# Optimization experiments

Hardware: AMD Instinct MI355X
Metric: run time of the kernel (lower is better)

The kernel has to match this reference:

```python
import jax, jax.numpy as jnp
import numpy as np
from jax import lax

SIZE = 20          # lattice half-extent in Angstrom
R = SIZE * 2       # 40 voxels per side (0.5 A pitch)
ROT = (1, 2, 3)    # fixed rot90 multiplicities (original draws randint(0,4,size=3))


def setup_inputs() -> dict:
    key = jax.random.key(0)
    ks = jax.random.split(key, 8)
    B, N1, N2, F = 8, 400, 64, 54
    # atom coordinates roughly inside the 20A box centered on the pocket
    pos1 = (jax.random.uniform(ks[0], (B, N1, 3)) - 0.5) * 18.0
    pos2 = (jax.random.uniform(ks[1], (B, N2, 3)) - 0.5) * 18.0
    h1 = jax.random.uniform(ks[2], (B, N1, F))
    h2 = jax.random.uniform(ks[3], (B, N2, F))
    valid1 = jnp.ones((B, N1), jnp.float32)
    valid2 = jnp.ones((B, N2), jnp.float32)
    conv_w = jax.random.normal(ks[4], (128, F, 3, 3, 3)) * 0.05
    conv_b = jnp.zeros((128,), jnp.float32)
    fc_w = jax.random.normal(ks[5], (128 * R * R * R, 1)) * 1e-3
    fc_b = jnp.zeros((1,), jnp.float32)
    return dict(pos1=pos1, pos2=pos2, h1=h1, h2=h2, valid1=valid1,
                valid2=valid2, conv_w=conv_w, conv_b=conv_b,
                fc_w=fc_w, fc_b=fc_b)


def _scatter_one(lat, idx, feat):
    # lat: [R+1,R+1,R+1,F] (extra slot R is the dump cell for out-of-range atoms)
    inb = jnp.all((idx >= 0) & (idx <= R - 1), axis=-1)          # [N]
    idxc = jnp.where(inb[:, None], idx, R)                       # route invalid -> R
    return lat.at[idxc[:, 0], idxc[:, 1], idxc[:, 2]].set(feat)


def _forward(pos1, pos2, h1, h2, valid1, valid2, conv_w, conv_b, fc_w, fc_b):
    B, _, F = h1.shape
    h1 = h1 * valid1[..., None]
    h2 = h2 * valid2[..., None]
    pos1 = pos1 * valid1[..., None]
    pos2 = pos2 * valid2[..., None]
    # per-batch bounding box of non-zero pos1 atoms -> box center `sub`
    nz = (pos1.sum(-1) == 0)[..., None]                          # [B,N1,1]
    bmax = jnp.max(pos1 + jnp.where(nz, -1e10, 0.0), axis=1)
    bmin = jnp.min(pos1 + jnp.where(nz, 1e10, 0.0), axis=1)
    sub = (bmin + (bmax - bmin) / 2)[:, None, :]                 # [B,1,3]
    half = jnp.float32(SIZE / 2)
    idx1 = jnp.floor((pos1 - sub + half) / 0.5).astype(jnp.int32)
    idx2 = jnp.floor((pos2 - sub + half) / 0.5).astype(jnp.int32)
    lat = jnp.zeros((B, R + 1, R + 1, R + 1, F), h1.dtype)
    lat = jax.vmap(_scatter_one)(lat, idx1, h1)                  # protein first
    lat = jax.vmap(_scatter_one)(lat, idx2, h2)                  # ligand overwrites
    lat = lat[:, :R, :R, :R, :]                                  # drop dump cell
    lat = jnp.transpose(lat, (0, 4, 2, 3, 1))                    # [B,F,y,z,x]
    lat = jnp.rot90(lat, k=ROT[0], axes=(2, 3))
    lat = jnp.rot90(lat, k=ROT[1], axes=(3, 4))
    lat = jnp.rot90(lat, k=ROT[2], axes=(4, 2))
    # ConvBlock: Conv3d(54,128,k=3,p=1) + ReLU (dropout disabled)
    y = lax.conv_general_dilated(lat, conv_w, (1, 1, 1), 'SAME',
                                 dimension_numbers=('NCDHW', 'OIDHW', 'NCDHW'))
    y = jax.nn.relu(y + conv_b[None, :, None, None, None])
    # PredictBlock: Linear(128*40^3, 1) + sigmoid
    y = y.reshape(B, -1)
    return jax.nn.sigmoid(y @ fc_w + fc_b)                       # [B,1]


def reference(pos1, pos2, h1, h2, valid1, valid2, conv_w, conv_b, fc_w, fc_b):
    return _forward(pos1, pos2, h1, h2, valid1, valid2,
                    conv_w, conv_b, fc_w, fc_b)
```

## Files before the change

kernel.cpp:

```cpp
#include <hip/hip_runtime.h>
#include <float.h>
#include <math.h>

constexpr int B = 8, N1 = 400, N2 = 64, NP = N1 + N2, F = 54, C = 128;
constexpr int RR = 40;
constexpr int RG = 41;
constexpr int VOX = RR*RR*RR;
constexpr int MAXOCC = NP;
constexpr int MAXACT = NP * 27;
constexpr int NBG = (VOX/64) * (C/16);
constexpr int PCHUNK = 16;
constexpr int NCHUNK = 32;
constexpr int BSR = 16384;
constexpr int PPS = 512;

constexpr size_t align256(size_t x) { return (x + 255) & ~(size_t)255; }

constexpr size_t OFF_SUB   = 0;
constexpr size_t OFF_WIN   = align256(OFF_SUB  + (size_t)B*3*4);
constexpr size_t SZ_WIN    = (size_t)B*RG*RG*RG*4;
constexpr size_t OFF_SLOT  = align256(OFF_WIN  + SZ_WIN);
constexpr size_t SZ_SLOT   = (size_t)B*VOX*4;
constexpr size_t OFF_AFST  = align256(OFF_SLOT + SZ_SLOT);
constexpr size_t FF_END    = OFF_AFST + SZ_SLOT;
constexpr size_t OFF_ACNTG = align256(FF_END);
constexpr size_t OFF_CNTS  = align256(OFF_ACNTG+ SZ_SLOT);
constexpr size_t OFF_BCNT  = align256(OFF_CNTS + (size_t)B*16*4);
constexpr size_t SZ_BCNT   = (size_t)B*27*16*4;
constexpr size_t Z_END     = OFF_BCNT + SZ_BCNT;
constexpr size_t OFF_OCC   = align256(Z_END);
constexpr size_t OFF_FEAT  = align256(OFF_OCC  + (size_t)B*MAXOCC*4);
constexpr size_t OFF_WT    = align256(OFF_FEAT + (size_t)B*MAXOCC*F*4);
constexpr size_t OFF_BG    = align256(OFF_WT   + (size_t)27*F*C*4);
constexpr size_t OFF_SBUK  = align256(OFF_BG   + (size_t)NBG*4);
constexpr size_t OFF_MLST  = align256(OFF_SBUK + (size_t)B*27*MAXOCC*8);
constexpr size_t OFF_BSUM  = align256(OFF_MLST + (size_t)B*MAXACT*8);
constexpr size_t OFF_FCT   = align256(OFF_BSUM + (size_t)B*BSR*4);
constexpr size_t OFF_END   = OFF_FCT + (size_t)VOX*C*4;

__global__ __launch_bounds__(64)
void k_init(const float* __restrict__ pos1, const float* __restrict__ valid1,
            float* __restrict__ sub, const float* __restrict__ conv_w,
            float* __restrict__ Wt) {
    if (blockIdx.x < B) {
        int b = blockIdx.x;
        int t = threadIdx.x;
        float bmax[3] = {-FLT_MAX, -FLT_MAX, -FLT_MAX};
        float bmin[3] = { FLT_MAX,  FLT_MAX,  FLT_MAX};
        for (int n = t; n < N1; n += 64) {
            float v = valid1[b*N1 + n];
            const float* pp = pos1 + ((size_t)b*N1 + n)*3;
            float p0 = pp[0]*v, p1 = pp[1]*v, p2 = pp[2]*v;
            float s = p0 + p1 + p2;
            bool nz = (s == 0.0f);
            float amax = nz ? -10000000000.0f : 0.0f;
            float amin = nz ?  10000000000.0f : 0.0f;
            bmax[0] = fmaxf(bmax[0], p0 + amax);
            bmax[1] = fmaxf(bmax[1], p1 + amax);
            bmax[2] = fmaxf(bmax[2], p2 + amax);
            bmin[0] = fminf(bmin[0], p0 + amin);
            bmin[1] = fminf(bmin[1], p1 + amin);
            bmin[2] = fminf(bmin[2], p2 + amin);
        }
        #pragma unroll
        for (int off = 32; off; off >>= 1) {
            #pragma unroll
            for (int d = 0; d < 3; d++) {
                bmax[d] = fmaxf(bmax[d], __shfl_xor(bmax[d], off));
                bmin[d] = fminf(bmin[d], __shfl_xor(bmin[d], off));
            }
        }
        if (t == 0) {
            #pragma unroll
            for (int d = 0; d < 3; d++)
                sub[b*3 + d] = bmin[d] + (bmax[d] - bmin[d]) / 2.0f;
        }
    } else {
        int g = (blockIdx.x - B)*64 + threadIdx.x;
        if (g < 27*F*C) {
            int o = g & (C-1);
            int rest = g >> 7;
            int f = rest % F, s = rest / F;
            Wt[g] = conv_w[((size_t)o*F + f)*27 + s];
        }
    }
}

__device__ inline void point_idx(const float* pos1, const float* valid1,
                                 const float* pos2, const float* valid2,
                                 const float* sub, int b, int n,
                                 int& ix, int& iy, int& iz, bool& inb, float& vout) {
    float px, py, pz, v;
    if (n < N1) {
        v = valid1[b*N1 + n];
        const float* p = pos1 + ((size_t)b*N1 + n)*3;
        px = p[0]*v; py = p[1]*v; pz = p[2]*v;
    } else {
        int m = n - N1;
        v = valid2[b*N2 + m];
        const float* p = pos2 + ((size_t)b*N2 + m)*3;
        px = p[0]*v; py = p[1]*v; pz = p[2]*v;
    }
    const float* sb = sub + b*3;
    ix = (int)floorf((px - sb[0] + 10.0f) / 0.5f);
    iy = (int)floorf((py - sb[1] + 10.0f) / 0.5f);
    iz = (int)floorf((pz - sb[2] + 10.0f) / 0.5f);
    inb = (ix >= 0 && ix <= RR-1 && iy >= 0 && iy <= RR-1 && iz >= 0 && iz <= RR-1);
    vout = v;
}

__global__ void k_scatter(const float* __restrict__ pos1, const float* __restrict__ valid1,
                          const float* __restrict__ pos2, const float* __restrict__ valid2,
                          const float* __restrict__ sub, int* __restrict__ winner) {
    int g = blockIdx.x*blockDim.x + threadIdx.x;
    if (g >= B*NP) return;
    int b = g / NP, n = g % NP;
    int ix, iy, iz; bool inb; float v;
    point_idx(pos1, valid1, pos2, valid2, sub, b, n, ix, iy, iz, inb, v);
    int x = inb ? ix : RR, y = inb ? iy : RR, z = inb ? iz : RR;
    int cell = (x*RG + y)*RG + z;
    atomicMax(&winner[(size_t)b*RG*RG*RG + cell], n);
}

__global__ void k_claim(const float* __restrict__ pos1, const float* __restrict__ valid1,
                        const float* __restrict__ pos2, const float* __restrict__ valid2,
                        const float* __restrict__ h1, const float* __restrict__ h2,
                        const float* __restrict__ sub, const int* __restrict__ winner,
                        int* __restrict__ slotGrid, int* __restrict__ counts,
                        int* __restrict__ occCoords, float* __restrict__ feats) {
    int g = blockIdx.x*blockDim.x + threadIdx.x;
    if (g >= B*NP) return;
    int b = g / NP, n = g % NP;
    int ix, iy, iz; bool inb; float v;
    point_idx(pos1, valid1, pos2, valid2, sub, b, n, ix, iy, iz, inb, v);
    if (!inb) return;
    int cell = (ix*RG + iy)*RG + iz;
    if (winner[(size_t)b*RG*RG*RG + cell] != n) return;
    int slot = atomicAdd(&counts[b*16], 1);
    slotGrid[(size_t)b*VOX + (ix*RR + iy)*RR + iz] = slot;
    occCoords[b*MAXOCC + slot] = (ix << 12) | (iy << 6) | iz;
    const float* h = (n < N1) ? (h1 + ((size_t)b*N1 + n)*F)
                              : (h2 + ((size_t)b*N2 + (n - N1))*F);
    float* fo = feats + ((size_t)b*MAXOCC + slot)*F;
    for (int f = 0; f < F; f++) fo[f] = h[f] * v;
}

__global__ void k_dilate(const int* __restrict__ counts, const int* __restrict__ occCoords,
                         int* __restrict__ actCnt, unsigned* __restrict__ actFirst) {
    int g = blockIdx.x*blockDim.x + threadIdx.x;
    if (g >= B*MAXOCC*27) return;
    int b = g / (MAXOCC*27);
    int rem = g % (MAXOCC*27);
    int sl = rem / 27, k = rem % 27;
    if (sl >= counts[b*16]) return;
    int pc = occCoords[b*MAXOCC + sl];
    int x = pc >> 12, y = (pc >> 6) & 63, z = pc & 63;
    int nx = x + k/9 - 1, ny = y + (k/3)%3 - 1, nz = z + k%3 - 1;
    if (nx < 0 || nx >= RR || ny < 0 || ny >= RR || nz < 0 || nz >= RR) return;
    size_t lin = (size_t)b*VOX + (nx*RR + ny)*RR + nz;
    atomicAdd(&actCnt[lin], 1);
    int sten = (2 - k/9)*9 + ((k/3)%3)*3 + (k%3);
    atomicMin(&actFirst[lin], ((unsigned)sl << 5) | (unsigned)sten);
}

__global__ __launch_bounds__(256)
void k_compact(const int* __restrict__ counts, const int* __restrict__ occCoords,
               const int* __restrict__ actCnt, const unsigned* __restrict__ actFirst,
               int* __restrict__ countsW, int* __restrict__ bCnt,
               int2* __restrict__ sBuck, int2* __restrict__ mList) {
    int g = blockIdx.x*256 + threadIdx.x;
    int bucket = g / PPS;
    int s = g % PPS;
    int b = bucket / 27, k = bucket % 27;
    if (b >= B) return;
    int sten = (2 - k/9)*9 + ((k/3)%3)*3 + (k%3);
    bool ownS = false, ownM = false; int pcOut = 0;
    if (s < counts[b*16]) {
        int pc = occCoords[b*MAXOCC + s];
        int x = pc >> 12, y = (pc >> 6) & 63, z = pc & 63;
        int x0 = x + k/9 - 1, y0 = y + (k/3)%3 - 1, z0 = z + k%3 - 1;
        if (x0 >= 0 && x0 < RR && y0 >= 0 && y0 < RR && z0 >= 0 && z0 < RR) {
            size_t lin = (size_t)b*VOX + (x0*RR + y0)*RR + z0;
            unsigned myid = ((unsigned)s << 5) | (unsigned)sten;
            if (actFirst[lin] == myid) {
                pcOut = (x0 << 12) | (y0 << 6) | z0;
                if (actCnt[lin] == 1) ownS = true; else ownM = true;
            }
        }
    }
    int lane = threadIdx.x & 63;
    unsigned long long mS = __ballot(ownS);
    if (mS != 0ull) {
        int lead = __builtin_ctzll(mS);
        int base = 0;
        if (lane == lead) base = atomicAdd(&bCnt[(b*27 + sten)*16], __popcll(mS));
        base = __shfl(base, lead);
        if (ownS) {
            int rank = __popcll(mS & ((1ull << lane) - 1ull));
            sBuck[((size_t)(b*27 + sten))*MAXOCC + base + rank] = make_int2(pcOut, s);
        }
    }
    unsigned long long mM = __ballot(ownM);
    if (mM != 0ull) {
        int lead = __builtin_ctzll(mM);
        int base = 0;
        if (lane == lead) base = atomicAdd(&countsW[b*16 + 8], __popcll(mM));
        base = __shfl(base, lead);
        if (ownM) {
            int rank = __popcll(mM & ((1ull << lane) - 1ull));
            mList[(size_t)b*MAXACT + base + rank] = make_int2(pcOut, 0);
        }
    }
}

__global__ __launch_bounds__(256)
void k_fct(const float* __restrict__ fc_w, const float* __restrict__ conv_b,
           float* __restrict__ fcT, float* __restrict__ bgBlock) {
    __shared__ float tile[16][65];
    __shared__ float sred[16][17];
    __shared__ float sredw[16];
    int v0 = blockIdx.x * 64;
    int o0 = blockIdx.y * 16;
    int t = threadIdx.x;
    int tv = t & 63, to = t >> 6;
    #pragma unroll
    for (int oo = 0; oo < 16; oo += 4)
        tile[to + oo][tv] = fc_w[(size_t)(o0 + to + oo)*VOX + v0 + tv];
    __syncthreads();
    int to2 = t & 15, tv2 = t >> 4;
    float s = 0.0f;
    #pragma unroll
    for (int vv = 0; vv < 64; vv += 16) {
        float val = tile[to2][tv2 + vv];
        fcT[(size_t)(v0 + tv2 + vv)*C + o0 + to2] = val;
        s += val;
    }
    sred[to2][tv2] = s;
    __syncthreads();
    if (t < 16) {
        float tot = 0.0f;
        #pragma unroll
        for (int i = 0; i < 16; i++) tot += sred[t][i];
        sredw[t] = fmaxf(conv_b[o0 + t], 0.0f) * tot;
    }
    __syncthreads();
    if (t == 0) {
        float tot = 0.0f;
        #pragma unroll
        for (int i = 0; i < 16; i++) tot += sredw[i];
        bgBlock[blockIdx.y*1000 + blockIdx.x] = tot;
    }
}

__global__ __launch_bounds__(256)
void k_bg_fb(const float* __restrict__ fc_w, const float* __restrict__ conv_b,
             float* __restrict__ bgBlock) {
    int o = blockIdx.x;
    int t = threadIdx.x;
    float s = 0.0f;
    for (int v = t; v < VOX; v += 256) s += fc_w[(size_t)o*VOX + v];
    #pragma unroll
    for (int off = 32; off; off >>= 1) s += __shfl_xor(s, off);
    __shared__ float red[4];
    if ((t & 63) == 0) red[t >> 6] = s;
    __syncthreads();
    if (t == 0) bgBlock[o] = fmaxf(conv_b[o], 0.0f) * (red[0] + red[1] + red[2] + red[3]);
}

__global__ __launch_bounds__(128)
void k_convS(const float* __restrict__ feats, const int* __restrict__ bCnt,
             const int2* __restrict__ sBuck, const float* __restrict__ Wt,
             const float* __restrict__ conv_b, const float* __restrict__ fcT,
             const float* __restrict__ fc_w, int useT, float* __restrict__ bsum) {
    int b = blockIdx.y;
    int sten = blockIdx.x >> 5;
    int chunk = blockIdx.x & 31;
    int t = threadIdx.x;
    int idxOut = sten*NCHUNK + chunk;
    int cnt = bCnt[(b*27 + sten)*16];
    int base = chunk*PCHUNK;
    if (base >= cnt) { if (t == 0) bsum[(size_t)b*BSR + idxOut] = 0.0f; return; }
    int rem = min(PCHUNK, cnt - base);

    __shared__ float fLDS[54][20];
    __shared__ int   flatS[16];
    __shared__ int   slotS[16];
    __shared__ float red[2];

    if (t < 16) {
        if (t < rem) {
            int2 e = sBuck[((size_t)(b*27 + sten))*MAXOCC + base + t];
            int pc = e.x;
            int x0 = pc >> 12, y0 = (pc >> 6) & 63, z0 = pc & 63;
            flatS[t] = x0*1600 + (RR-1 - y0)*RR + (RR-1 - z0);
            slotS[t] = e.y;
        } else { flatS[t] = 0; slotS[t] = -1; }
    }
    __syncthreads();
    for (int idx = t; idx < PCHUNK*F; idx += 128) {
        int p = idx / F, f = idx - p*F;
        int sl = slotS[p];
        fLDS[f][p] = (sl >= 0) ? feats[((size_t)b*MAXOCC + sl)*F + f] : 0.0f;
    }
    __syncthreads();

    const float* wv = Wt + (size_t)sten*F*C + t;
    float acc[16];
    #pragma unroll
    for (int p = 0; p < 16; p++) acc[p] = 0.0f;
    #pragma unroll 3
    for (int f = 0; f < F; f++) {
        float w = wv[(size_t)f*C];
        float4 a = *(const float4*)&fLDS[f][0];
        float4 q = *(const float4*)&fLDS[f][4];
        float4 c = *(const float4*)&fLDS[f][8];
        float4 d = *(const float4*)&fLDS[f][12];
        acc[0]  = fmaf(a.x, w, acc[0]);  acc[1]  = fmaf(a.y, w, acc[1]);
        acc[2]  = fmaf(a.z, w, acc[2]);  acc[3]  = fmaf(a.w, w, acc[3]);
        acc[4]  = fmaf(q.x, w, acc[4]);  acc[5]  = fmaf(q.y, w, acc[5]);
        acc[6]  = fmaf(q.z, w, acc[6]);  acc[7]  = fmaf(q.w, w, acc[7]);
        acc[8]  = fmaf(c.x, w, acc[8]);  acc[9]  = fmaf(c.y, w, acc[9]);
        acc[10] = fmaf(c.z, w, acc[10]); acc[11] = fmaf(c.w, w, acc[11]);
        acc[12] = fmaf(d.x, w, acc[12]); acc[13] = fmaf(d.y, w, acc[13]);
        acc[14] = fmaf(d.z, w, acc[14]); acc[15] = fmaf(d.w, w, acc[15]);
    }
    float cb = conv_b[t];
    float rb = fmaxf(cb, 0.0f);
    float ssum = 0.0f;
    #pragma unroll
    for (int p = 0; p < 16; p++) {
        if (p < rem) {
            float outv = fmaxf(acc[p] + cb, 0.0f) - rb;
            float wf = useT ? fcT[(size_t)flatS[p]*C + t]
                            : fc_w[(size_t)t*VOX + flatS[p]];
            ssum = fmaf(outv, wf, ssum);
        }
    }
    #pragma unroll
    for (int off = 32; off; off >>= 1) ssum += __shfl_xor(ssum, off);
    if ((t & 63) == 0) red[t >> 6] = ssum;
    __syncthreads();
    if (t == 0) bsum[(size_t)b*BSR + idxOut] = red[0] + red[1];
}

__global__ __launch_bounds__(256)
void k_convM(const int* __restrict__ slotGrid, const float* __restrict__ feats,
             const int* __restrict__ counts, const int2* __restrict__ mList,
             const float* __restrict__ Wt, const float* __restrict__ conv_b,
             const float* __restrict__ fcT, const float* __restrict__ fc_w, int useT,
             float* __restrict__ bsum) {
    int b = blockIdx.y;
    int wave = blockIdx.x*4 + (threadIdx.x >> 6);
    int lane = threadIdx.x & 63;
    int cntM = counts[b*16 + 8];
    int nw = gridDim.x*4;
    float cb0 = conv_b[lane], cb1 = conv_b[lane + 64];
    float rb0 = fmaxf(cb0, 0.0f), rb1 = fmaxf(cb1, 0.0f);

    for (int i = wave; i < cntM; i += nw) {
        int pc = mList[(size_t)b*MAXACT + i].x;
        int x0 = pc >> 12, y0 = (pc >> 6) & 63, z0 = pc & 63;
        int sl = -1;
        if (lane < 27) {
            int dp = lane/9, dq = (lane/3)%3, dr = lane%3;
            int nx = x0 + dp - 1, ny = y0 + 1 - dq, nz = z0 + 1 - dr;
            if (nx >= 0 && nx < RR && ny >= 0 && ny < RR && nz >= 0 && nz < RR)
                sl = slotGrid[(size_t)b*VOX + (nx*RR + ny)*RR + nz];
        }
        unsigned long long mask = __ballot(sl >= 0);
        float acc0 = 0.0f, acc1 = 0.0f;
        while (mask) {
            int eA = __builtin_ctzll(mask); mask &= mask - 1;
            int eB = eA;
            bool two = (mask != 0ull);
            if (two) { eB = __builtin_ctzll(mask); mask &= mask - 1; }
            int slA = __shfl(sl, eA);
            int slB = __shfl(sl, eB);
            float v0 = 0.0f, v1 = 0.0f;
            if (lane < F) {
                v0 = feats[((size_t)b*MAXOCC + slA)*F + lane];
                v1 = two ? feats[((size_t)b*MAXOCC + slB)*F + lane] : 0.0f;
            }
            const float* wpA = Wt + (size_t)eA*F*C;
            const float* wpB = Wt + (size_t)eB*F*C;
            #pragma unroll 9
            for (int f = 0; f < F; f++) {
                float fA = __shfl(v0, f);
                float fB = __shfl(v1, f);
                acc0 = fmaf(fA, wpA[f*C + lane],      acc0);
                acc1 = fmaf(fA, wpA[f*C + lane + 64], acc1);
                acc0 = fmaf(fB, wpB[f*C + lane],      acc0);
                acc1 = fmaf(fB, wpB[f*C + lane + 64], acc1);
            }
        }
        float o0 = fmaxf(acc0 + cb0, 0.0f) - rb0;
        float o1 = fmaxf(acc1 + cb1, 0.0f) - rb1;
        int flat = x0*1600 + (RR-1 - y0)*RR + (RR-1 - z0);
        float w0, w1;
        if (useT) {
            w0 = fcT[(size_t)flat*C + lane];
            w1 = fcT[(size_t)flat*C + lane + 64];
        } else {
            w0 = fc_w[(size_t)lane*VOX + flat];
            w1 = fc_w[(size_t)(lane + 64)*VOX + flat];
        }
        float s = fmaf(o0, w0, o1*w1);
        #pragma unroll
        for (int off = 32; off; off >>= 1) s += __shfl_xor(s, off);
        if (lane == 0) bsum[(size_t)b*BSR + 1024 + i] = s;
    }
}

__global__ __launch_bounds__(1024)
void k_reduce(const float* __restrict__ bsum, const float* __restrict__ bgBlock,
              const float* __restrict__ fc_b, const int* __restrict__ counts,
              float* __restrict__ out) {
    int b = blockIdx.x;
    int t = threadIdx.x;
    float s = 0.0f;
    for (int i = t; i < 27*NCHUNK; i += 1024) s += bsum[(size_t)b*BSR + i];
    int cntM = counts[b*16 + 8];
    for (int i = t; i < cntM; i += 1024) s += bsum[(size_t)b*BSR + 1024 + i];
    for (int i = t; i < NBG; i += 1024) s += bgBlock[i];
    #pragma unroll
    for (int off = 32; off; off >>= 1) s += __shfl_xor(s, off);
    __shared__ float red[16];
    if ((t & 63) == 0) red[t >> 6] = s;
    __syncthreads();
    if (t == 0) {
        float tot = fc_b[0];
        #pragma unroll
        for (int i = 0; i < 16; i++) tot += red[i];
        out[b] = 1.0f / (1.0f + expf(-tot));
    }
}

extern "C" void kernel_launch(void* const* d_in, const int* in_sizes, int n_in,
                              void* d_out, int out_size, void* d_ws, size_t ws_size,
                              hipStream_t stream) {
    const float* pos1   = (const float*)d_in[0];
    const float* pos2   = (const float*)d_in[1];
    const float* h1     = (const float*)d_in[2];
    const float* h2     = (const float*)d_in[3];
    const float* valid1 = (const float*)d_in[4];
    const float* valid2 = (const float*)d_in[5];
    const float* conv_w = (const float*)d_in[6];
    const float* conv_b = (const float*)d_in[7];
    const float* fc_w   = (const float*)d_in[8];
    const float* fc_b   = (const float*)d_in[9];
    float* out = (float*)d_out;

    char* ws = (char*)d_ws;
    float*    sub      = (float*)   (ws + OFF_SUB);
    int*      winner   = (int*)     (ws + OFF_WIN);
    int*      slotGrid = (int*)     (ws + OFF_SLOT);
    unsigned* actFirst = (unsigned*)(ws + OFF_AFST);
    int*      actCnt   = (int*)     (ws + OFF_ACNTG);
    int*      counts   = (int*)     (ws + OFF_CNTS);
    int*      bCnt     = (int*)     (ws + OFF_BCNT);
    int*      occCoords= (int*)     (ws + OFF_OCC);
    float*    feats    = (float*)   (ws + OFF_FEAT);
    float*    Wt       = (float*)   (ws + OFF_WT);
    float*    bgBlock  = (float*)   (ws + OFF_BG);
    int2*     sBuck    = (int2*)    (ws + OFF_SBUK);
    int2*     mList    = (int2*)    (ws + OFF_MLST);
    float*    bsum     = (float*)   (ws + OFF_BSUM);
    float*    fcT      = (float*)   (ws + OFF_FCT);

    const int useT = (ws_size >= OFF_END) ? 1 : 0;

    hipMemsetAsync(ws + OFF_WIN,   0xFF, FF_END - OFF_WIN,   stream);
    hipMemsetAsync(ws + OFF_ACNTG, 0x00, Z_END - OFF_ACNTG,  stream);

    k_init<<<B + (27*F*C + 63)/64, 64, 0, stream>>>(pos1, valid1, sub, conv_w, Wt);
    k_scatter<<<(B*NP + 255)/256, 256, 0, stream>>>(pos1, valid1, pos2, valid2, sub, winner);
    k_claim<<<(B*NP + 255)/256, 256, 0, stream>>>(pos1, valid1, pos2, valid2, h1, h2,
                                                  sub, winner, slotGrid, counts, occCoords, feats);
    k_dilate<<<(B*MAXOCC*27 + 255)/256, 256, 0, stream>>>(counts, occCoords, actCnt, actFirst);
    k_compact<<<(B*27*PPS)/256, 256, 0, stream>>>(counts, occCoords, actCnt, actFirst,
                                                  counts, bCnt, sBuck, mList);
    if (useT) {
        k_fct<<<dim3(VOX/64, C/16), 256, 0, stream>>>(fc_w, conv_b, fcT, bgBlock);
    } else {
        hipMemsetAsync(bgBlock, 0x00, (size_t)NBG*4, stream);
        k_bg_fb<<<C, 256, 0, stream>>>(fc_w, conv_b, bgBlock);
    }
    k_convS<<<dim3(27*NCHUNK, B), 128, 0, stream>>>(feats, bCnt, sBuck, Wt, conv_b,
                                                    fcT, fc_w, useT, bsum);
    k_convM<<<dim3(512, B), 256, 0, stream>>>(slotGrid, feats, counts, mList,
                                              Wt, conv_b, fcT, fc_w, useT, bsum);
    k_reduce<<<B, 1024, 0, stream>>>(bsum, bgBlock, fc_b, counts, out);
}
```

Baseline: 130.2 us.

## Merge sparse conv kernels into one launch with LDS-staged weights

```diff
diff --git a/kernel.cpp b/kernel.cpp
--- a/kernel.cpp
+++ b/kernel.cpp
@@ -11,6 +11,9 @@
 constexpr int NBG = (VOX/64) * (C/16);
 constexpr int PCHUNK = 16;
 constexpr int NCHUNK = 32;
+constexpr int NQ = 4;
+constexpr int SBLK = 27*NQ;
+constexpr int MBLK = 384;
 constexpr int BSR = 16384;
 constexpr int PPS = 512;
 
@@ -267,134 +270,121 @@
     if (t == 0) bgBlock[o] = fmaxf(conv_b[o], 0.0f) * (red[0] + red[1] + red[2] + red[3]);
 }
 
-__global__ __launch_bounds__(128)
-void k_convS(const float* __restrict__ feats, const int* __restrict__ bCnt,
-             const int2* __restrict__ sBuck, const float* __restrict__ Wt,
-             const float* __restrict__ conv_b, const float* __restrict__ fcT,
-             const float* __restrict__ fc_w, int useT, float* __restrict__ bsum) {
-    int b = blockIdx.y;
-    int sten = blockIdx.x >> 5;
-    int chunk = blockIdx.x & 31;
-    int t = threadIdx.x;
-    int idxOut = sten*NCHUNK + chunk;
-    int cnt = bCnt[(b*27 + sten)*16];
-    int base = chunk*PCHUNK;
-    if (base >= cnt) { if (t == 0) bsum[(size_t)b*BSR + idxOut] = 0.0f; return; }
-    int rem = min(PCHUNK, cnt - base);
-
-    __shared__ float fLDS[54][20];
-    __shared__ int   flatS[16];
-    __shared__ int   slotS[16];
-    __shared__ float red[2];
-
-    if (t < 16) {
-        if (t < rem) {
-            int2 e = sBuck[((size_t)(b*27 + sten))*MAXOCC + base + t];
-            int pc = e.x;
-            int x0 = pc >> 12, y0 = (pc >> 6) & 63, z0 = pc & 63;
-            flatS[t] = x0*1600 + (RR-1 - y0)*RR + (RR-1 - z0);
-            slotS[t] = e.y;
-        } else { flatS[t] = 0; slotS[t] = -1; }
-    }
-    __syncthreads();
-    for (int idx = t; idx < PCHUNK*F; idx += 128) {
-        int p = idx / F, f = idx - p*F;
-        int sl = slotS[p];
-        fLDS[f][p] = (sl >= 0) ? feats[((size_t)b*MAXOCC + sl)*F + f] : 0.0f;
-    }
-    __syncthreads();
-
-    const float* wv = Wt + (size_t)sten*F*C + t;
-    float acc[16];
-    #pragma unroll
-    for (int p = 0; p < 16; p++) acc[p] = 0.0f;
-    #pragma unroll 3
-    for (int f = 0; f < F; f++) {
-        float w = wv[(size_t)f*C];
-        float4 a = *(const float4*)&fLDS[f][0];
-        float4 q = *(const float4*)&fLDS[f][4];
-        float4 c = *(const float4*)&fLDS[f][8];
-        float4 d = *(const float4*)&fLDS[f][12];
-        acc[0]  = fmaf(a.x, w, acc[0]);  acc[1]  = fmaf(a.y, w, acc[1]);
-        acc[2]  = fmaf(a.z, w, acc[2]);  acc[3]  = fmaf(a.w, w, acc[3]);
-        acc[4]  = fmaf(q.x, w, acc[4]);  acc[5]  = fmaf(q.y, w, acc[5]);
-        acc[6]  = fmaf(q.z, w, acc[6]);  acc[7]  = fmaf(q.w, w, acc[7]);
-        acc[8]  = fmaf(c.x, w, acc[8]);  acc[9]  = fmaf(c.y, w, acc[9]);
-        acc[10] = fmaf(c.z, w, acc[10]); acc[11] = fmaf(c.w, w, acc[11]);
-        acc[12] = fmaf(d.x, w, acc[12]); acc[13] = fmaf(d.y, w, acc[13]);
-        acc[14] = fmaf(d.z, w, acc[14]); acc[15] = fmaf(d.w, w, acc[15]);
-    }
-    float cb = conv_b[t];
-    float rb = fmaxf(cb, 0.0f);
-    float ssum = 0.0f;
-    #pragma unroll
-    for (int p = 0; p < 16; p++) {
-        if (p < rem) {
-            float outv = fmaxf(acc[p] + cb, 0.0f) - rb;
-            float wf = useT ? fcT[(size_t)flatS[p]*C + t]
-                            : fc_w[(size_t)t*VOX + flatS[p]];
-            ssum = fmaf(outv, wf, ssum);
-        }
-    }
-    #pragma unroll
-    for (int off = 32; off; off >>= 1) ssum += __shfl_xor(ssum, off);
-    if ((t & 63) == 0) red[t >> 6] = ssum;
-    __syncthreads();
-    if (t == 0) bsum[(size_t)b*BSR + idxOut] = red[0] + red[1];
-}
-
 __global__ __launch_bounds__(256)
-void k_convM(const int* __restrict__ slotGrid, const float* __restrict__ feats,
-             const int* __restrict__ counts, const int2* __restrict__ mList,
+void k_conv2(const int* __restrict__ slotGrid, const float* __restrict__ feats,
+             const int* __restrict__ counts, const int* __restrict__ bCnt,
+             const int2* __restrict__ sBuck, const int2* __restrict__ mList,
              const float* __restrict__ Wt, const float* __restrict__ conv_b,
              const float* __restrict__ fcT, const float* __restrict__ fc_w, int useT,
              float* __restrict__ bsum) {
     int b = blockIdx.y;
-    int wave = blockIdx.x*4 + (threadIdx.x >> 6);
-    int lane = threadIdx.x & 63;
+    int t = threadIdx.x;
+
+    __shared__ float wlds[F*C];
+    __shared__ float fl[F][20];
+    __shared__ int   flatS[16];
+    __shared__ int   slotS[16];
+    __shared__ float red[4];
+
+    if (blockIdx.x < SBLK) {
+        int sten = blockIdx.x >> 2;
+        int q    = blockIdx.x & 3;
+        int ch = t & 127, ph = t >> 7;
+        int cnt = bCnt[(b*27 + sten)*16];
+
+        if (t == 0) {
+            for (int c = q; c < NCHUNK; c += NQ)
+                if (c*PCHUNK >= cnt) bsum[(size_t)b*BSR + sten*NCHUNK + c] = 0.0f;
+        }
+        if (cnt <= q*PCHUNK) return;
+
+        const float* wg = Wt + (size_t)sten*F*C;
+        #pragma unroll
+        for (int i = 0; i < F*C/256; i++) wlds[i*256 + t] = wg[i*256 + t];
+
+        float cb = conv_b[ch];
+        float rb = fmaxf(cb, 0.0f);
+
+        for (int c = q; c < NCHUNK; c += NQ) {
+            int base = c*PCHUNK;
+            if (base >= cnt) break;
+            int rem = min(PCHUNK, cnt - base);
+            __syncthreads();
+            if (t < 16) {
+                if (t < rem) {
+                    int2 e = sBuck[((size_t)(b*27 + sten))*MAXOCC + base + t];
+                    int pc = e.x;
+                    int x0 = pc >> 12, y0 = (pc >> 6) & 63, z0 = pc & 63;
+                    flatS[t] = x0*1600 + (RR-1 - y0)*RR + (RR-1 - z0);
+                    slotS[t] = e.y;
+                } else { flatS[t] = 0; slotS[t] = -1; }
+            }
+            __syncthreads();
+            float wf0, wf1, wf2, wf3, wf4, wf5, wf6, wf7;
+            {
+                int p0 = ph*8;
+                if (useT) {
+                    wf0 = fcT[(size_t)flatS[p0+0]*C + ch]; wf1 = fcT[(size_t)flatS[p0+1]*C + ch];
+                    wf2 = fcT[(size_t)flatS[p0+2]*C + ch]; wf3 = fcT[(size_t)flatS[p0+3]*C + ch];
+                    wf4 = fcT[(size_t)flatS[p0+4]*C + ch]; wf5 = fcT[(size_t)flatS[p0+5]*C + ch];
+                    wf6 = fcT[(size_t)flatS[p0+6]*C + ch]; wf7 = fcT[(size_t)flatS[p0+7]*C + ch];
+                } else {
+                    const float* fw = fc_w + (size_t)ch*VOX;
+                    wf0 = fw[flatS[p0+0]]; wf1 = fw[flatS[p0+1]];
+                    wf2 = fw[flatS[p0+2]]; wf3 = fw[flatS[p0+3]];
+                    wf4 = fw[flatS[p0+4]]; wf5 = fw[flatS[p0+5]];
+                    wf6 = fw[flatS[p0+6]]; wf7 = fw[flatS[p0+7]];
+                }
+            }
+            for (int idx = t; idx < PCHUNK*F; idx += 256) {
+                int p = idx / F, f = idx - p*F;
+                int sl = slotS[p];
+                fl[f][p] = (sl >= 0) ? feats[((size_t)b*MAXOCC + sl)*F + f] : 0.0f;
+            }
+            __syncthreads();
+
+            float a0=0,a1=0,a2=0,a3=0,a4=0,a5=0,a6=0,a7=0;
+            #pragma unroll 6
+            for (int f = 0; f < F; f++) {
+                float w = wlds[f*C + ch];
+                float4 u = *(const float4*)&fl[f][ph*8 + 0];
+                float4 v = *(const float4*)&fl[f][ph*8 + 4];
+                a0 = fmaf(u.x, w, a0); a1 = fmaf(u.y, w, a1);
+                a2 = fmaf(u.z, w, a2); a3 = fmaf(u.w, w, a3);
+                a4 = fmaf(v.x, w, a4); a5 = fmaf(v.y, w, a5);
+                a6 = fmaf(v.z, w, a6); a7 = fmaf(v.w, w, a7);
+            }
+            float ssum =
+                fmaf(fmaxf(a0 + cb, 0.0f) - rb, wf0,
+                fmaf(fmaxf(a1 + cb, 0.0f) - rb, wf1,
+                fmaf(fmaxf(a2 + cb, 0.0f) - rb, wf2,
+                fmaf(fmaxf(a3 + cb, 0.0f) - rb, wf3,
+                fmaf(fmaxf(a4 + cb, 0.0f) - rb, wf4,
+                fmaf(fmaxf(a5 + cb, 0.0f) - rb, wf5,
+                fmaf(fmaxf(a6 + cb, 0.0f) - rb, wf6,
+                     (fmaxf(a7 + cb, 0.0f) - rb) * wf7)))))));
+            #pragma unroll
+            for (int off = 32; off; off >>= 1) ssum += __shfl_xor(ssum, off);
+            if ((t & 63) == 0) red[t >> 6] = ssum;
+            __syncthreads();
+            if (t == 0)
+                bsum[(size_t)b*BSR + sten*NCHUNK + c] = red[0] + red[1] + red[2] + red[3];
+        }
+        return;
+    }
+
+    int mb = blockIdx.x - SBLK;
+    int wave = mb*4 + (t >> 6);
+    int lane = t & 63;
     int cntM = counts[b*16 + 8];
-    int nw = gridDim.x*4;
+    int nw = MBLK*4;
     float cb0 = conv_b[lane], cb1 = conv_b[lane + 64];
     float rb0 = fmaxf(cb0, 0.0f), rb1 = fmaxf(cb1, 0.0f);
+    const float* fb = feats + (size_t)b*MAXOCC*F;
 
     for (int i = wave; i < cntM; i += nw) {
         int pc = mList[(size_t)b*MAXACT + i].x;
         int x0 = pc >> 12, y0 = (pc >> 6) & 63, z0 = pc & 63;
-        int sl = -1;
-        if (lane < 27) {
-            int dp = lane/9, dq = (lane/3)%3, dr = lane%3;
-            int nx = x0 + dp - 1, ny = y0 + 1 - dq, nz = z0 + 1 - dr;
-            if (nx >= 0 && nx < RR && ny >= 0 && ny < RR && nz >= 0 && nz < RR)
-                sl = slotGrid[(size_t)b*VOX + (nx*RR + ny)*RR + nz];
-        }
-        unsigned long long mask = __ballot(sl >= 0);
-        float acc0 = 0.0f, acc1 = 0.0f;
-        while (mask) {
-            int eA = __builtin_ctzll(mask); mask &= mask - 1;
-            int eB = eA;
-            bool two = (mask != 0ull);
-            if (two) { eB = __builtin_ctzll(mask); mask &= mask - 1; }
-            int slA = __shfl(sl, eA);
-            int slB = __shfl(sl, eB);
-            float v0 = 0.0f, v1 = 0.0f;
-            if (lane < F) {
-                v0 = feats[((size_t)b*MAXOCC + slA)*F + lane];
-                v1 = two ? feats[((size_t)b*MAXOCC + slB)*F + lane] : 0.0f;
-            }
-            const float* wpA = Wt + (size_t)eA*F*C;
-            const float* wpB = Wt + (size_t)eB*F*C;
-            #pragma unroll 9
-            for (int f = 0; f < F; f++) {
-                float fA = __shfl(v0, f);
-                float fB = __shfl(v1, f);
-                acc0 = fmaf(fA, wpA[f*C + lane],      acc0);
-                acc1 = fmaf(fA, wpA[f*C + lane + 64], acc1);
-                acc0 = fmaf(fB, wpB[f*C + lane],      acc0);
-                acc1 = fmaf(fB, wpB[f*C + lane + 64], acc1);
-            }
-        }
-        float o0 = fmaxf(acc0 + cb0, 0.0f) - rb0;
-        float o1 = fmaxf(acc1 + cb1, 0.0f) - rb1;
         int flat = x0*1600 + (RR-1 - y0)*RR + (RR-1 - z0);
         float w0, w1;
         if (useT) {
@@ -404,6 +394,50 @@
             w0 = fc_w[(size_t)lane*VOX + flat];
             w1 = fc_w[(size_t)(lane + 64)*VOX + flat];
         }
+        int sl = -1;
+        if (lane < 27) {
+            int dp = lane/9, dq = (lane/3)%3, dr = lane%3;
+            int nx = x0 + dp - 1, ny = y0 + 1 - dq, nz = z0 + 1 - dr;
+            if (nx >= 0 && nx < RR && ny >= 0 && ny < RR && nz >= 0 && nz < RR)
+                sl = slotGrid[(size_t)b*VOX + (nx*RR + ny)*RR + nz];
+        }
+        unsigned long long mask = __ballot(sl >= 0);
+        float acc0 = 0.0f, acc1 = 0.0f;
+        while (mask) {
+            int eA = __builtin_ctzll(mask); mask &= mask - 1;
+            int eB = eA, eC = eA, eD = eA, n = 1;
+            if (mask) { eB = __builtin_ctzll(mask); mask &= mask - 1; n = 2;
+              if (mask) { eC = __builtin_ctzll(mask); mask &= mask - 1; n = 3;
+                if (mask) { eD = __builtin_ctzll(mask); mask &= mask - 1; n = 4; } } }
+            int slA = __shfl(sl, eA), slB = __shfl(sl, eB);
+            int slC = __shfl(sl, eC), slD = __shfl(sl, eD);
+            float v0 = 0.0f, v1 = 0.0f, v2 = 0.0f, v3 = 0.0f;
+            if (lane < F) {
+                v0 = fb[(size_t)slA*F + lane];
+                v1 = (n > 1) ? fb[(size_t)slB*F + lane] : 0.0f;
+                v2 = (n > 2) ? fb[(size_t)slC*F + lane] : 0.0f;
+                v3 = (n > 3) ? fb[(size_t)slD*F + lane] : 0.0f;
+            }
+            const float* wpA = Wt + (size_t)eA*F*C;
+            const float* wpB = Wt + (size_t)eB*F*C;
+            const float* wpC = Wt + (size_t)eC*F*C;
+            const float* wpD = Wt + (size_t)eD*F*C;
+            #pragma unroll 6
+            for (int f = 0; f < F; f++) {
+                float fA = __shfl(v0, f), fB = __shfl(v1, f);
+                float fC = __shfl(v2, f), fD = __shfl(v3, f);
+                acc0 = fmaf(fA, wpA[f*C + lane],      acc0);
+                acc1 = fmaf(fA, wpA[f*C + lane + 64], acc1);
+                acc0 = fmaf(fB, wpB[f*C + lane],      acc0);
+                acc1 = fmaf(fB, wpB[f*C + lane + 64], acc1);
+                acc0 = fmaf(fC, wpC[f*C + lane],      acc0);
+                acc1 = fmaf(fC, wpC[f*C + lane + 64], acc1);
+                acc0 = fmaf(fD, wpD[f*C + lane],      acc0);
+                acc1 = fmaf(fD, wpD[f*C + lane + 64], acc1);
+            }
+        }
+        float o0 = fmaxf(acc0 + cb0, 0.0f) - rb0;
+        float o1 = fmaxf(acc1 + cb1, 0.0f) - rb1;
         float s = fmaf(o0, w0, o1*w1);
         #pragma unroll
         for (int off = 32; off; off >>= 1) s += __shfl_xor(s, off);
@@ -485,9 +519,8 @@
         hipMemsetAsync(bgBlock, 0x00, (size_t)NBG*4, stream);
         k_bg_fb<<<C, 256, 0, stream>>>(fc_w, conv_b, bgBlock);
     }
-    k_convS<<<dim3(27*NCHUNK, B), 128, 0, stream>>>(feats, bCnt, sBuck, Wt, conv_b,
-                                                    fcT, fc_w, useT, bsum);
-    k_convM<<<dim3(512, B), 256, 0, stream>>>(slotGrid, feats, counts, mList,
-                                              Wt, conv_b, fcT, fc_w, useT, bsum);
+    k_conv2<<<dim3(SBLK + MBLK, B), 256, 0, stream>>>(slotGrid, feats, counts, bCnt,
+                                                      sBuck, mList, Wt, conv_b,
+                                                      fcT, fc_w, useT, bsum);
     k_reduce<<<B, 1024, 0, stream>>>(bsum, bgBlock, fc_b, counts, out);
 }
```

Result: slower. 138.3 us (+6.3%).

## Add transposed padded weights, widen convS point chunks, batch four stencil taps in convM

Applied to the files above, without the earlier changes.

```diff
diff --git a/kernel.cpp b/kernel.cpp
--- a/kernel.cpp
+++ b/kernel.cpp
@@ -3,14 +3,15 @@
 #include <math.h>
 
 constexpr int B = 8, N1 = 400, N2 = 64, NP = N1 + N2, F = 54, C = 128;
+constexpr int FP = 56;
 constexpr int RR = 40;
 constexpr int RG = 41;
 constexpr int VOX = RR*RR*RR;
 constexpr int MAXOCC = NP;
 constexpr int MAXACT = NP * 27;
 constexpr int NBG = (VOX/64) * (C/16);
-constexpr int PCHUNK = 16;
-constexpr int NCHUNK = 32;
+constexpr int PCHUNK = 32;
+constexpr int NCHUNK = 16;
 constexpr int BSR = 16384;
 constexpr int PPS = 512;
 
@@ -31,17 +32,21 @@
 constexpr size_t OFF_OCC   = align256(Z_END);
 constexpr size_t OFF_FEAT  = align256(OFF_OCC  + (size_t)B*MAXOCC*4);
 constexpr size_t OFF_WT    = align256(OFF_FEAT + (size_t)B*MAXOCC*F*4);
-constexpr size_t OFF_BG    = align256(OFF_WT   + (size_t)27*F*C*4);
+constexpr size_t OFF_WTT   = align256(OFF_WT   + (size_t)27*F*C*4);
+constexpr size_t OFF_BG    = align256(OFF_WTT  + (size_t)27*C*FP*4);
 constexpr size_t OFF_SBUK  = align256(OFF_BG   + (size_t)NBG*4);
 constexpr size_t OFF_MLST  = align256(OFF_SBUK + (size_t)B*27*MAXOCC*8);
 constexpr size_t OFF_BSUM  = align256(OFF_MLST + (size_t)B*MAXACT*8);
 constexpr size_t OFF_FCT   = align256(OFF_BSUM + (size_t)B*BSR*4);
 constexpr size_t OFF_END   = OFF_FCT + (size_t)VOX*C*4;
 
+constexpr int WT_BLKS  = (27*F*C + 63)/64;
+constexpr int WTT_BLKS = (27*C*FP + 63)/64;
+
 __global__ __launch_bounds__(64)
 void k_init(const float* __restrict__ pos1, const float* __restrict__ valid1,
             float* __restrict__ sub, const float* __restrict__ conv_w,
-            float* __restrict__ Wt) {
+            float* __restrict__ Wt, float* __restrict__ WtT) {
     if (blockIdx.x < B) {
         int b = blockIdx.x;
         int t = threadIdx.x;
@@ -75,13 +80,21 @@
             for (int d = 0; d < 3; d++)
                 sub[b*3 + d] = bmin[d] + (bmax[d] - bmin[d]) / 2.0f;
         }
-    } else {
+    } else if (blockIdx.x < B + WT_BLKS) {
         int g = (blockIdx.x - B)*64 + threadIdx.x;
         if (g < 27*F*C) {
             int o = g & (C-1);
             int rest = g >> 7;
             int f = rest % F, s = rest / F;
             Wt[g] = conv_w[((size_t)o*F + f)*27 + s];
+        }
+    } else {
+        int g = (blockIdx.x - B - WT_BLKS)*64 + threadIdx.x;
+        if (g < 27*C*FP) {
+            int f = g % FP;
+            int rest = g / FP;
+            int c = rest & (C-1), s = rest >> 7;
+            WtT[g] = (f < F) ? conv_w[((size_t)c*F + f)*27 + s] : 0.0f;
         }
     }
 }
@@ -269,25 +282,25 @@
 
 __global__ __launch_bounds__(128)
 void k_convS(const float* __restrict__ feats, const int* __restrict__ bCnt,
-             const int2* __restrict__ sBuck, const float* __restrict__ Wt,
+             const int2* __restrict__ sBuck, const float* __restrict__ WtT,
              const float* __restrict__ conv_b, const float* __restrict__ fcT,
              const float* __restrict__ fc_w, int useT, float* __restrict__ bsum) {
     int b = blockIdx.y;
-    int sten = blockIdx.x >> 5;
-    int chunk = blockIdx.x & 31;
+    int sten = blockIdx.x >> 4;
+    int chunk = blockIdx.x & 15;
     int t = threadIdx.x;
-    int idxOut = sten*NCHUNK + chunk;
+    int idxOut = blockIdx.x;
     int cnt = bCnt[(b*27 + sten)*16];
     int base = chunk*PCHUNK;
     if (base >= cnt) { if (t == 0) bsum[(size_t)b*BSR + idxOut] = 0.0f; return; }
     int rem = min(PCHUNK, cnt - base);
 
-    __shared__ float fLDS[54][20];
-    __shared__ int   flatS[16];
-    __shared__ int   slotS[16];
+    __shared__ __align__(16) float fl[FP*32];
+    __shared__ int   flatS[32];
+    __shared__ int   slotS[32];
     __shared__ float red[2];
 
-    if (t < 16) {
+    if (t < 32) {
         if (t < rem) {
             int2 e = sBuck[((size_t)(b*27 + sten))*MAXOCC + base + t];
             int pc = e.x;
@@ -297,44 +310,57 @@
         } else { flatS[t] = 0; slotS[t] = -1; }
     }
     __syncthreads();
-    for (int idx = t; idx < PCHUNK*F; idx += 128) {
-        int p = idx / F, f = idx - p*F;
+    #pragma unroll
+    for (int it = 0; it < FP*32/128; it++) {
+        int idx = it*128 + t;
+        int p = idx & 31, f = idx >> 5;
         int sl = slotS[p];
-        fLDS[f][p] = (sl >= 0) ? feats[((size_t)b*MAXOCC + sl)*F + f] : 0.0f;
-    }
-    __syncthreads();
-
-    const float* wv = Wt + (size_t)sten*F*C + t;
-    float acc[16];
-    #pragma unroll
-    for (int p = 0; p < 16; p++) acc[p] = 0.0f;
-    #pragma unroll 3
-    for (int f = 0; f < F; f++) {
-        float w = wv[(size_t)f*C];
-        float4 a = *(const float4*)&fLDS[f][0];
-        float4 q = *(const float4*)&fLDS[f][4];
-        float4 c = *(const float4*)&fLDS[f][8];
-        float4 d = *(const float4*)&fLDS[f][12];
-        acc[0]  = fmaf(a.x, w, acc[0]);  acc[1]  = fmaf(a.y, w, acc[1]);
-        acc[2]  = fmaf(a.z, w, acc[2]);  acc[3]  = fmaf(a.w, w, acc[3]);
-        acc[4]  = fmaf(q.x, w, acc[4]);  acc[5]  = fmaf(q.y, w, acc[5]);
-        acc[6]  = fmaf(q.z, w, acc[6]);  acc[7]  = fmaf(q.w, w, acc[7]);
-        acc[8]  = fmaf(c.x, w, acc[8]);  acc[9]  = fmaf(c.y, w, acc[9]);
-        acc[10] = fmaf(c.z, w, acc[10]); acc[11] = fmaf(c.w, w, acc[11]);
-        acc[12] = fmaf(d.x, w, acc[12]); acc[13] = fmaf(d.y, w, acc[13]);
-        acc[14] = fmaf(d.z, w, acc[14]); acc[15] = fmaf(d.w, w, acc[15]);
-    }
+        fl[idx] = (sl >= 0 && f < F) ? feats[((size_t)b*MAXOCC + sl)*F + f] : 0.0f;
+    }
+    __syncthreads();
+
+    const float4* wrow = (const float4*)(WtT + ((size_t)sten*C + t)*FP);
+    float4 acc4[8];
+    #pragma unroll
+    for (int i = 0; i < 8; i++) acc4[i] = make_float4(0.f, 0.f, 0.f, 0.f);
+
+    for (int j = 0; j < FP/4; j++) {
+        float4 wq = wrow[j];
+        #pragma unroll
+        for (int k = 0; k < 4; k++) {
+            float w = (k == 0) ? wq.x : (k == 1) ? wq.y : (k == 2) ? wq.z : wq.w;
+            const float4* fp = (const float4*)&fl[(j*4 + k)*32];
+            #pragma unroll
+            for (int i = 0; i < 8; i++) {
+                float4 u = fp[i];
+                acc4[i].x = fmaf(u.x, w, acc4[i].x);
+                acc4[i].y = fmaf(u.y, w, acc4[i].y);
+                acc4[i].z = fmaf(u.z, w, acc4[i].z);
+                acc4[i].w = fmaf(u.w, w, acc4[i].w);
+            }
+        }
+    }
+
     float cb = conv_b[t];
     float rb = fmaxf(cb, 0.0f);
     float ssum = 0.0f;
     #pragma unroll
-    for (int p = 0; p < 16; p++) {
-        if (p < rem) {
-            float outv = fmaxf(acc[p] + cb, 0.0f) - rb;
-            float wf = useT ? fcT[(size_t)flatS[p]*C + t]
-                            : fc_w[(size_t)t*VOX + flatS[p]];
-            ssum = fmaf(outv, wf, ssum);
-        }
+    for (int i = 0; i < 8; i++) {
+        float wf0, wf1, wf2, wf3;
+        if (useT) {
+            wf0 = fcT[(size_t)flatS[4*i+0]*C + t];
+            wf1 = fcT[(size_t)flatS[4*i+1]*C + t];
+            wf2 = fcT[(size_t)flatS[4*i+2]*C + t];
+            wf3 = fcT[(size_t)flatS[4*i+3]*C + t];
+        } else {
+            const float* fw = fc_w + (size_t)t*VOX;
+            wf0 = fw[flatS[4*i+0]]; wf1 = fw[flatS[4*i+1]];
+            wf2 = fw[flatS[4*i+2]]; wf3 = fw[flatS[4*i+3]];
+        }
+        ssum = fmaf(fmaxf(acc4[i].x + cb, 0.0f) - rb, wf0, ssum);
+        ssum = fmaf(fmaxf(acc4[i].y + cb, 0.0f) - rb, wf1, ssum);
+        ssum = fmaf(fmaxf(acc4[i].z + cb, 0.0f) - rb, wf2, ssum);
+        ssum = fmaf(fmaxf(acc4[i].w + cb, 0.0f) - rb, wf3, ssum);
     }
     #pragma unroll
     for (int off = 32; off; off >>= 1) ssum += __shfl_xor(ssum, off);
@@ -356,45 +382,11 @@
     int nw = gridDim.x*4;
     float cb0 = conv_b[lane], cb1 = conv_b[lane + 64];
     float rb0 = fmaxf(cb0, 0.0f), rb1 = fmaxf(cb1, 0.0f);
+    const float* fb = feats + (size_t)b*MAXOCC*F;
 
     for (int i = wave; i < cntM; i += nw) {
         int pc = mList[(size_t)b*MAXACT + i].x;
         int x0 = pc >> 12, y0 = (pc >> 6) & 63, z0 = pc & 63;
-        int sl = -1;
-        if (lane < 27) {
-            int dp = lane/9, dq = (lane/3)%3, dr = lane%3;
-            int nx = x0 + dp - 1, ny = y0 + 1 - dq, nz = z0 + 1 - dr;
-            if (nx >= 0 && nx < RR && ny >= 0 && ny < RR && nz >= 0 && nz < RR)
-                sl = slotGrid[(size_t)b*VOX + (nx*RR + ny)*RR + nz];
-        }
-        unsigned long long mask = __ballot(sl >= 0);
-        float acc0 = 0.0f, acc1 = 0.0f;
-        while (mask) {
-            int eA = __builtin_ctzll(mask); mask &= mask - 1;
-            int eB = eA;
-            bool two = (mask != 0ull);
-            if (two) { eB = __builtin_ctzll(mask); mask &= mask - 1; }
-            int slA = __shfl(sl, eA);
-            int slB = __shfl(sl, eB);
-            float v0 = 0.0f, v1 = 0.0f;
-            if (lane < F) {
-                v0 = feats[((size_t)b*MAXOCC + slA)*F + lane];
-                v1 = two ? feats[((size_t)b*MAXOCC + slB)*F + lane] : 0.0f;
-            }
-            const float* wpA = Wt + (size_t)eA*F*C;
-            const float* wpB = Wt + (size_t)eB*F*C;
-            #pragma unroll 9
-            for (int f = 0; f < F; f++) {
-                float fA = __shfl(v0, f);
-                float fB = __shfl(v1, f);
-                acc0 = fmaf(fA, wpA[f*C + lane],      acc0);
-                acc1 = fmaf(fA, wpA[f*C + lane + 64], acc1);
-                acc0 = fmaf(fB, wpB[f*C + lane],      acc0);
-                acc1 = fmaf(fB, wpB[f*C + lane + 64], acc1);
-            }
-        }
-        float o0 = fmaxf(acc0 + cb0, 0.0f) - rb0;
-        float o1 = fmaxf(acc1 + cb1, 0.0f) - rb1;
         int flat = x0*1600 + (RR-1 - y0)*RR + (RR-1 - z0);
         float w0, w1;
         if (useT) {
@@ -404,6 +396,50 @@
             w0 = fc_w[(size_t)lane*VOX + flat];
             w1 = fc_w[(size_t)(lane + 64)*VOX + flat];
         }
+        int sl = -1;
+        if (lane < 27) {
+            int dp = lane/9, dq = (lane/3)%3, dr = lane%3;
+            int nx = x0 + dp - 1, ny = y0 + 1 - dq, nz = z0 + 1 - dr;
+            if (nx >= 0 && nx < RR && ny >= 0 && ny < RR && nz >= 0 && nz < RR)
+                sl = slotGrid[(size_t)b*VOX + (nx*RR + ny)*RR + nz];
+        }
+        unsigned long long mask = __ballot(sl >= 0);
+        float acc0 = 0.0f, acc1 = 0.0f;
+        while (mask) {
+            int eA = __builtin_ctzll(mask); mask &= mask - 1;
+            int eB = eA, eC = eA, eD = eA, n = 1;
+            if (mask) { eB = __builtin_ctzll(mask); mask &= mask - 1; n = 2;
+              if (mask) { eC = __builtin_ctzll(mask); mask &= mask - 1; n = 3;
+                if (mask) { eD = __builtin_ctzll(mask); mask &= mask - 1; n = 4; } } }
+            int slA = __shfl(sl, eA), slB = __shfl(sl, eB);
+            int slC = __shfl(sl, eC), slD = __shfl(sl, eD);
+            float v0 = 0.0f, v1 = 0.0f, v2 = 0.0f, v3 = 0.0f;
+            if (lane < F) {
+                v0 = fb[(size_t)slA*F + lane];
+                v1 = (n > 1) ? fb[(size_t)slB*F + lane] : 0.0f;
+                v2 = (n > 2) ? fb[(size_t)slC*F + lane] : 0.0f;
+                v3 = (n > 3) ? fb[(size_t)slD*F + lane] : 0.0f;
+            }
+            const float* wpA = Wt + (size_t)eA*F*C;
+            const float* wpB = Wt + (size_t)eB*F*C;
+            const float* wpC = Wt + (size_t)eC*F*C;
+            const float* wpD = Wt + (size_t)eD*F*C;
+            #pragma unroll 6
+            for (int f = 0; f < F; f++) {
+                float fA = __shfl(v0, f), fB = __shfl(v1, f);
+                float fC = __shfl(v2, f), fD = __shfl(v3, f);
+                acc0 = fmaf(fA, wpA[f*C + lane],      acc0);
+                acc1 = fmaf(fA, wpA[f*C + lane + 64], acc1);
+                acc0 = fmaf(fB, wpB[f*C + lane],      acc0);
+                acc1 = fmaf(fB, wpB[f*C + lane + 64], acc1);
+                acc0 = fmaf(fC, wpC[f*C + lane],      acc0);
+                acc1 = fmaf(fC, wpC[f*C + lane + 64], acc1);
+                acc0 = fmaf(fD, wpD[f*C + lane],      acc0);
+                acc1 = fmaf(fD, wpD[f*C + lane + 64], acc1);
+            }
+        }
+        float o0 = fmaxf(acc0 + cb0, 0.0f) - rb0;
+        float o1 = fmaxf(acc1 + cb1, 0.0f) - rb1;
         float s = fmaf(o0, w0, o1*w1);
         #pragma unroll
         for (int off = 32; off; off >>= 1) s += __shfl_xor(s, off);
@@ -461,6 +497,7 @@
     int*      occCoords= (int*)     (ws + OFF_OCC);
     float*    feats    = (float*)   (ws + OFF_FEAT);
     float*    Wt       = (float*)   (ws + OFF_WT);
+    float*    WtT      = (float*)   (ws + OFF_WTT);
     float*    bgBlock  = (float*)   (ws + OFF_BG);
     int2*     sBuck    = (int2*)    (ws + OFF_SBUK);
     int2*     mList    = (int2*)    (ws + OFF_MLST);
@@ -472,7 +509,7 @@
     hipMemsetAsync(ws + OFF_WIN,   0xFF, FF_END - OFF_WIN,   stream);
     hipMemsetAsync(ws + OFF_ACNTG, 0x00, Z_END - OFF_ACNTG,  stream);
 
-    k_init<<<B + (27*F*C + 63)/64, 64, 0, stream>>>(pos1, valid1, sub, conv_w, Wt);
+    k_init<<<B + WT_BLKS + WTT_BLKS, 64, 0, stream>>>(pos1, valid1, sub, conv_w, Wt, WtT);
     k_scatter<<<(B*NP + 255)/256, 256, 0, stream>>>(pos1, valid1, pos2, valid2, sub, winner);
     k_claim<<<(B*NP + 255)/256, 256, 0, stream>>>(pos1, valid1, pos2, valid2, h1, h2,
                                                   sub, winner, slotGrid, counts, occCoords, feats);
@@ -485,7 +522,7 @@
         hipMemsetAsync(bgBlock, 0x00, (size_t)NBG*4, stream);
         k_bg_fb<<<C, 256, 0, stream>>>(fc_w, conv_b, bgBlock);
     }
-    k_convS<<<dim3(27*NCHUNK, B), 128, 0, stream>>>(feats, bCnt, sBuck, Wt, conv_b,
+    k_convS<<<dim3(27*NCHUNK, B), 128, 0, stream>>>(feats, bCnt, sBuck, WtT, conv_b,
                                                     fcT, fc_w, useT, bsum);
     k_convM<<<dim3(512, B), 256, 0, stream>>>(slotGrid, feats, counts, mList,
                                               Wt, conv_b, fcT, fc_w, useT, bsum);
```

Result: slower. 149.5 us (+14.8%).
